# Kernel optimization log

Measured on AMD Instinct MI355X. Metric: run time of the kernel, lower is better.

The kernel has to match this reference:

```python
import jax, jax.numpy as jnp
import numpy as np

B, S, D = 1, 4096, 2048
H, KV, HD = 16, 4, 128
GROUPS = H // KV
SCALE = HD ** -0.5
ROPE_BASE = 10000.0
NEG = -1e9


def _rope_tables():
    inv_freq = 1.0 / (ROPE_BASE ** (jnp.arange(0, HD, 2, dtype=jnp.float32) / HD))  # [HD/2]
    pos = jnp.arange(S, dtype=jnp.float32)
    freqs = pos[:, None] * inv_freq[None, :]            # [S, HD/2]
    emb = jnp.concatenate([freqs, freqs], axis=-1)      # [S, HD] (HF convention)
    return jnp.cos(emb)[None], jnp.sin(emb)[None]       # [1, S, HD]


def setup_inputs() -> dict:
    key = jax.random.key(0)
    ks = jax.random.split(key, 6)
    cos, sin = _rope_tables()
    causal = jnp.tril(jnp.ones((S, S), dtype=bool))
    attention_mask = jnp.where(causal, 0.0, NEG).astype(jnp.float32)[None, None]  # [1,1,S,S]
    std = 0.02
    return {
        "hidden_states": jax.random.normal(ks[0], (B, S, D), jnp.float32),
        "cos": cos.astype(jnp.float32),
        "sin": sin.astype(jnp.float32),
        "attention_mask": attention_mask,
        "wq": jax.random.normal(ks[1], (H * HD, D), jnp.float32) * std,
        "wk": jax.random.normal(ks[2], (KV * HD, D), jnp.float32) * std,
        "wv": jax.random.normal(ks[3], (KV * HD, D), jnp.float32) * std,
        "wo": jax.random.normal(ks[4], (D, H * HD), jnp.float32) * std,
    }


def _rotate_half(x):
    x1, x2 = x[..., : HD // 2], x[..., HD // 2:]
    return jnp.concatenate([-x2, x1], axis=-1)


def reference(hidden_states, cos, sin, attention_mask, wq, wk, wv, wo):
    b, s, _ = hidden_states.shape
    # projections -> [B, n_heads, S, HD]
    q = (hidden_states @ wq.T).reshape(b, s, H, HD).transpose(0, 2, 1, 3)
    k = (hidden_states @ wk.T).reshape(b, s, KV, HD).transpose(0, 2, 1, 3)
    v = (hidden_states @ wv.T).reshape(b, s, KV, HD).transpose(0, 2, 1, 3)
    # RoPE (HF apply_rotary_pos_emb, unsqueeze head dim)
    c, sn = cos[:, None], sin[:, None]
    q = q * c + _rotate_half(q) * sn
    k = k * c + _rotate_half(k) * sn
    # GQA: repeat kv heads
    k = jnp.repeat(k, GROUPS, axis=1)
    v = jnp.repeat(v, GROUPS, axis=1)
    # eager attention
    scores = jnp.einsum("bhqd,bhkd->bhqk", q, k) * SCALE + attention_mask
    attn = jax.nn.softmax(scores, axis=-1)
    out = jnp.einsum("bhqk,bhkd->bhqd", attn, v)
    out = out.transpose(0, 2, 1, 3).reshape(b, s, H * HD)
    # output projection (all-reduce is identity at world_size=1)
    return out @ wo.T
```

## Files before the change

kernel.cpp:

```cpp
#include <hip/hip_runtime.h>
#include <hip/hip_bf16.h>

#define SEQ   4096
#define DMODEL 2048
#define NHEAD 16
#define NKVH  4
#define HDIM  128
#define NQ    (NHEAD*HDIM)
#define NKV   (NKVH*HDIM)
#define NQKV  (NQ + 2*NKV)
#define SCALE 0.08838834764831845f
#define LOG2E 1.4426950408889634f
#define SCL2  (SCALE * LOG2E)

typedef __bf16 bf16x4 __attribute__((ext_vector_type(4)));
typedef __bf16 bf16x8 __attribute__((ext_vector_type(8)));
typedef float  f32x4  __attribute__((ext_vector_type(4)));

#define GLOBAL_CPTR(x) ((const __attribute__((address_space(1))) void*)(x))
#define LDS_PTR(x)     ((__attribute__((address_space(3))) void*)(x))

__global__ __launch_bounds__(256)
void convert_kernel(__bf16* __restrict__ dst, const float* __restrict__ src, int n8)
{
    const int i = blockIdx.x * 256 + threadIdx.x;
    if (i >= n8) return;
    const size_t e0 = (size_t)i * 8;
    const float4 a = *(const float4*)(src + e0);
    const float4 b = *(const float4*)(src + e0 + 4);
    bf16x8 o;
    o[0]=(__bf16)a.x; o[1]=(__bf16)a.y; o[2]=(__bf16)a.z; o[3]=(__bf16)a.w;
    o[4]=(__bf16)b.x; o[5]=(__bf16)b.y; o[6]=(__bf16)b.z; o[7]=(__bf16)b.w;
    *(bf16x8*)(dst + e0) = o;
}

__global__ __launch_bounds__(256)
void gemm_bt(const __bf16* __restrict__ A, const __bf16* __restrict__ Bw,
             void* __restrict__ Cv, __bf16* __restrict__ kb2, __bf16* __restrict__ vt2,
             const float* __restrict__ ct, const float* __restrict__ st,
             int M, int N, int K, int cmode)
{
    __shared__ alignas(16) __bf16 As[2][128*32];
    __shared__ alignas(16) __bf16 Bs[2][128*32];

    const int tid  = threadIdx.x;
    const int w    = tid >> 6;
    const int lane = tid & 63;
    const int l16  = lane & 15;
    const int quad = lane >> 4;
    const int m0 = blockIdx.y * 128;
    const int n0 = blockIdx.x * 128;

    const int srow = lane >> 2;
    const int scol = (lane & 3) * 8;

    const int wm = (w >> 1) * 64;
    int coff[4];
    #pragma unroll
    for (int nt = 0; nt < 4; ++nt)
        coff[nt] = (cmode == 3) ? ((w & 1) * 32 + ((nt & 2) ? 64 : 0) + (nt & 1) * 16)
                                : ((w & 1) * 64 + nt * 16);

    f32x4 acc[4][4];
    #pragma unroll
    for (int mt = 0; mt < 4; ++mt)
        #pragma unroll
        for (int nt = 0; nt < 4; ++nt)
            acc[mt][nt] = (f32x4){0.f, 0.f, 0.f, 0.f};

    auto STAGE = [&](int k0, int b) {
        #pragma unroll
        for (int c = 0; c < 2; ++c) {
            const int r0 = w * 32 + c * 16;
            const __bf16* ga = A + (size_t)(m0 + r0 + srow) * K + k0 + scol;
            __builtin_amdgcn_global_load_lds(GLOBAL_CPTR(ga), LDS_PTR(&As[b][r0 * 32]), 16, 0, 0);
            const __bf16* gb = Bw + (size_t)(n0 + r0 + srow) * K + k0 + scol;
            __builtin_amdgcn_global_load_lds(GLOBAL_CPTR(gb), LDS_PTR(&Bs[b][r0 * 32]), 16, 0, 0);
        }
    };

    STAGE(0, 0);
    for (int k0 = 0; k0 < K; k0 += 32) {
        const int b = (k0 >> 5) & 1;
        __syncthreads();
        if (k0 + 32 < K) STAGE(k0 + 32, b ^ 1);

        bf16x8 af[4], bf[4];
        #pragma unroll
        for (int mt = 0; mt < 4; ++mt)
            af[mt] = *(const bf16x8*)&As[b][(wm + mt*16 + l16) * 32 + quad * 8];
        #pragma unroll
        for (int nt = 0; nt < 4; ++nt)
            bf[nt] = *(const bf16x8*)&Bs[b][(coff[nt] + l16) * 32 + quad * 8];
        __builtin_amdgcn_s_setprio(1);
        #pragma unroll
        for (int mt = 0; mt < 4; ++mt)
            #pragma unroll
            for (int nt = 0; nt < 4; ++nt)
                acc[mt][nt] = __builtin_amdgcn_mfma_f32_16x16x32_bf16(
                    af[mt], bf[nt], acc[mt][nt], 0, 0, 0);
        __builtin_amdgcn_s_setprio(0);
    }

    if (cmode == 3) {
        if (n0 >= 2560) {
            #pragma unroll
            for (int mt = 0; mt < 4; ++mt)
                #pragma unroll
                for (int nt = 0; nt < 4; ++nt) {
                    const int col = (n0 - 2560) + coff[nt] + l16;
                    const int row = m0 + wm + mt*16 + quad*4;
                    bf16x4 pk;
                    #pragma unroll
                    for (int r = 0; r < 4; ++r) pk[r] = (__bf16)acc[mt][nt][r];
                    *(bf16x4*)&vt2[(size_t)col * M + row] = pk;
                }
        } else {
            __bf16* dst;
            int ncols, cb;
            if (n0 < 2048) { dst = (__bf16*)Cv; ncols = NQ;  cb = n0; }
            else           { dst = kb2;         ncols = NKV; cb = n0 - 2048; }
            #pragma unroll
            for (int mt = 0; mt < 4; ++mt)
                #pragma unroll
                for (int np = 0; np < 2; ++np) {
                    const int d = coff[np] + l16;
                    #pragma unroll
                    for (int r = 0; r < 4; ++r) {
                        const int s = m0 + wm + mt*16 + quad*4 + r;
                        const float c  = ct[s * HDIM + d];
                        const float sn = st[s * HDIM + d];
                        const float x1 = acc[mt][np][r];
                        const float x2 = acc[mt][np + 2][r];
                        dst[(size_t)s * ncols + cb + d]      = (__bf16)(x1 * c - x2 * sn);
                        dst[(size_t)s * ncols + cb + d + 64] = (__bf16)(x2 * c + x1 * sn);
                    }
                }
        }
    } else if (cmode == 1) {
        float* Cf = (float*)Cv;
        #pragma unroll
        for (int mt = 0; mt < 4; ++mt)
            #pragma unroll
            for (int nt = 0; nt < 4; ++nt) {
                const int row = m0 + wm + mt*16 + quad*4;
                const int col = n0 + coff[nt] + l16;
                #pragma unroll
                for (int r = 0; r < 4; ++r)
                    Cf[(size_t)(row + r) * N + col] = acc[mt][nt][r];
            }
    } else {
        __bf16* Cb = (__bf16*)Cv;
        #pragma unroll
        for (int mt = 0; mt < 4; ++mt)
            #pragma unroll
            for (int nt = 0; nt < 4; ++nt) {
                const int row = m0 + wm + mt*16 + quad*4;
                const int col = n0 + coff[nt] + l16;
                #pragma unroll
                for (int r = 0; r < 4; ++r)
                    Cb[(size_t)(row + r) * N + col] = (__bf16)acc[mt][nt][r];
            }
    }
}

__global__ __launch_bounds__(512, 4)
void attn_kernel(__bf16* __restrict__ QO, const __bf16* __restrict__ Kb,
                 const __bf16* __restrict__ Vt)
{
    __shared__ alignas(16) __bf16 Klds[2][4][64][32];
    __shared__ alignas(16) __bf16 Vlds[2][2][128][32];
    __shared__ alignas(16) __bf16 Ps[8][16][64];

    const int tid  = threadIdx.x;
    const int w    = tid >> 6;
    const int lane = tid & 63;
    const int l16  = lane & 15;
    const int quad = lane >> 4;
    const int bx = (int)blockIdx.x;
    const int h  = (int)blockIdx.y;
    const int g  = h >> 2;
    const int nbx = (int)gridDim.x;
    const int qt = (h < 8) ? (nbx - 1 - bx) : bx;
    const int m0 = qt * 128;
    const int wrow = m0 + w * 16;

    const int srow = lane >> 2;
    const int scol = (((lane & 3) ^ ((lane >> 3) & 3)) * 8);
    const int rsw  = (quad ^ ((l16 >> 1) & 3)) * 8;

    const int kcw = w & 3;
    const int hw  = w >> 2;

    bf16x8 qf[4];
    {
        const size_t qbase = (size_t)(wrow + l16) * NQ + h * HDIM;
        #pragma unroll
        for (int kc = 0; kc < 4; ++kc)
            qf[kc] = *(const bf16x8*)&QO[qbase + kc * 32 + quad * 8];
    }

    bf16x8 onesf;
    #pragma unroll
    for (int i = 0; i < 8; ++i) onesf[i] = (__bf16)1.0f;

    const __bf16* kSrc = Kb + (size_t)(hw * 32 + srow) * NKV + g * HDIM + kcw * 32 + scol;
    const __bf16* vSrc = Vt + (size_t)(g * HDIM + kcw * 32 + srow) * SEQ + hw * 32 + scol;

    auto STAGE = [&](int jj, int b) {
        const int n0g = jj * 64;
        #pragma unroll
        for (int c = 0; c < 2; ++c) {
            __builtin_amdgcn_global_load_lds(
                GLOBAL_CPTR(kSrc + (size_t)(n0g + c * 16) * NKV),
                LDS_PTR(&Klds[b][kcw][hw * 32 + c * 16][0]), 16, 0, 0);
            __builtin_amdgcn_global_load_lds(
                GLOBAL_CPTR(vSrc + (size_t)(c * 16) * SEQ + n0g),
                LDS_PTR(&Vlds[b][hw][kcw * 32 + c * 16][0]), 16, 0, 0);
        }
    };

    f32x4 lacc = (f32x4){0.f, 0.f, 0.f, 0.f};
    f32x4 oacc[8];
    #pragma unroll
    for (int t = 0; t < 8; ++t) oacc[t] = (f32x4){0.f, 0.f, 0.f, 0.f};

    const int njt = 2 * qt + 2;
    STAGE(0, 0);
    for (int j = 0; j < njt; ++j) {
        __syncthreads();
        if (j + 1 < njt) STAGE(j + 1, (j + 1) & 1);
        const int n0g = j * 64;
        if (n0g > wrow + 15) continue;
        const int b = j & 1;

        f32x4 sacc[4];
        #pragma unroll
        for (int nt = 0; nt < 4; ++nt) sacc[nt] = (f32x4){0.f, 0.f, 0.f, 0.f};
        __builtin_amdgcn_s_setprio(1);
        #pragma unroll
        for (int kc = 0; kc < 4; ++kc) {
            #pragma unroll
            for (int nt = 0; nt < 4; ++nt) {
                const bf16x8 kf = *(const bf16x8*)&Klds[b][kc][nt * 16 + l16][rsw];
                sacc[nt] = __builtin_amdgcn_mfma_f32_16x16x32_bf16(qf[kc], kf, sacc[nt], 0, 0, 0);
            }
        }
        __builtin_amdgcn_s_setprio(0);

        const bool needmask = (n0g + 64 > wrow);
        #pragma unroll
        for (int r = 0; r < 4; ++r) {
            const int qr = wrow + quad * 4 + r;
            const int prow = quad * 4 + r;
            const int pxor = (prow & 7) << 3;
            #pragma unroll
            for (int nt = 0; nt < 4; ++nt) {
                float e = exp2f(sacc[nt][r] * SCL2);
                if (needmask && (n0g + nt * 16 + l16) > qr) e = 0.f;
                Ps[w][prow][(nt * 16 + l16) ^ pxor] = (__bf16)e;
            }
        }

        bf16x8 pa[2];
        #pragma unroll
        for (int kc = 0; kc < 2; ++kc)
            pa[kc] = *(const bf16x8*)&Ps[w][l16][(kc * 32 + quad * 8) ^ ((l16 & 7) << 3)];

        __builtin_amdgcn_s_setprio(1);
        lacc = __builtin_amdgcn_mfma_f32_16x16x32_bf16(pa[0], onesf, lacc, 0, 0, 0);
        lacc = __builtin_amdgcn_mfma_f32_16x16x32_bf16(pa[1], onesf, lacc, 0, 0, 0);
        #pragma unroll
        for (int kc = 0; kc < 2; ++kc)
            #pragma unroll
            for (int t = 0; t < 8; ++t) {
                const bf16x8 vf = *(const bf16x8*)&Vlds[b][kc][t * 16 + l16][rsw];
                oacc[t] = __builtin_amdgcn_mfma_f32_16x16x32_bf16(pa[kc], vf, oacc[t], 0, 0, 0);
            }
        __builtin_amdgcn_s_setprio(0);
    }

    float rinv[4];
    #pragma unroll
    for (int r = 0; r < 4; ++r) rinv[r] = 1.f / lacc[r];
    #pragma unroll
    for (int t = 0; t < 8; ++t)
        #pragma unroll
        for (int r = 0; r < 4; ++r) {
            const int qr = wrow + quad * 4 + r;
            QO[(size_t)qr * NQ + h * HDIM + t * 16 + l16] = (__bf16)(oacc[t][r] * rinv[r]);
        }
}

extern "C" void kernel_launch(void* const* d_in, const int* in_sizes, int n_in,
                              void* d_out, int out_size, void* d_ws, size_t ws_size,
                              hipStream_t stream)
{
    const float* hidden = (const float*)d_in[0];
    const float* cosp   = (const float*)d_in[1];
    const float* sinp   = (const float*)d_in[2];
    const float* wq = (const float*)d_in[4];
    const float* wk = (const float*)d_in[5];
    const float* wv = (const float*)d_in[6];
    const float* wo = (const float*)d_in[7];

    const size_t nw_q = (size_t)NQ  * DMODEL;
    const size_t nw_k = (size_t)NKV * DMODEL;
    const size_t nq_e = (size_t)SEQ * NQ;
    const size_t nk_e = (size_t)SEQ * NKV;

    __bf16* ws     = (__bf16*)d_ws;
    __bf16* wo_b   = ws;
    __bf16* wqkv_b = wo_b + nw_q;
    __bf16* qbuf   = wqkv_b + nw_q + 2 * nw_k;
    __bf16* kbuf   = qbuf + nq_e;
    __bf16* vtb    = kbuf + nk_e;
    __bf16* hbuf   = (__bf16*)d_out;

    const dim3 blk(256);
    convert_kernel<<<dim3(nw_q / 8 / 256), blk, 0, stream>>>(wqkv_b, wq, nw_q / 8);
    convert_kernel<<<dim3(nw_k / 8 / 256), blk, 0, stream>>>(wqkv_b + nw_q, wk, nw_k / 8);
    convert_kernel<<<dim3(nw_k / 8 / 256), blk, 0, stream>>>(wqkv_b + nw_q + nw_k, wv, nw_k / 8);
    convert_kernel<<<dim3(nw_q / 8 / 256), blk, 0, stream>>>(wo_b, wo, nw_q / 8);
    convert_kernel<<<dim3(nq_e / 8 / 256), blk, 0, stream>>>(hbuf, hidden, nq_e / 8);

    gemm_bt<<<dim3(NQKV / 128, SEQ / 128), blk, 0, stream>>>(
        hbuf, wqkv_b, qbuf, kbuf, vtb, cosp, sinp, SEQ, NQKV, DMODEL, 3);

    attn_kernel<<<dim3(SEQ / 128, NHEAD), dim3(512), 0, stream>>>(qbuf, kbuf, vtb);

    gemm_bt<<<dim3(DMODEL / 128, SEQ / 128), blk, 0, stream>>>(
        qbuf, wo_b, d_out, nullptr, nullptr, nullptr, nullptr, SEQ, DMODEL, DMODEL, 1);
}
```

Before: 431.3 us.

## Fuse conversion launches, swizzle GEMM LDS tiles, split attention mask path

Merges the five fp32-to-bf16 conversion launches into one kernel that picks its source and destination from the block index. Adds an XOR swizzle on the GEMM shared-memory staging and fragment reads to reduce LDS bank conflicts. Splits the attention softmax into a masked path for diagonal tiles and an unmasked path for the rest, which removes per-element compare work on most tiles. Drops the unused bf16 GEMM epilogue.

After: 412.7 us. 4.3% less time.

```diff
diff --git a/kernel.cpp b/kernel.cpp
--- a/kernel.cpp
+++ b/kernel.cpp
@@ -21,16 +21,27 @@
 #define LDS_PTR(x)     ((__attribute__((address_space(3))) void*)(x))
 
 __global__ __launch_bounds__(256)
-void convert_kernel(__bf16* __restrict__ dst, const float* __restrict__ src, int n8)
+void convert_all(__bf16* __restrict__ wqkv, __bf16* __restrict__ wob,
+                 __bf16* __restrict__ hb,
+                 const float* __restrict__ wq, const float* __restrict__ wk,
+                 const float* __restrict__ wv, const float* __restrict__ wo,
+                 const float* __restrict__ hid)
 {
-    const int i = blockIdx.x * 256 + threadIdx.x;
-    if (i >= n8) return;
-    const size_t e0 = (size_t)i * 8;
+    const int b = blockIdx.x;
+    const float* src;
+    __bf16* dst;
+    int ib;
+    if (b < 2048)      { src = wq;  dst = wqkv;                                 ib = b; }
+    else if (b < 2560) { src = wk;  dst = wqkv + (size_t)NQ * DMODEL;           ib = b - 2048; }
+    else if (b < 3072) { src = wv;  dst = wqkv + (size_t)(NQ + NKV) * DMODEL;   ib = b - 2560; }
+    else if (b < 5120) { src = wo;  dst = wob;                                  ib = b - 3072; }
+    else               { src = hid; dst = hb;                                   ib = b - 5120; }
+    const size_t e0 = ((size_t)ib * 256 + threadIdx.x) * 8;
     const float4 a = *(const float4*)(src + e0);
-    const float4 b = *(const float4*)(src + e0 + 4);
+    const float4 c = *(const float4*)(src + e0 + 4);
     bf16x8 o;
     o[0]=(__bf16)a.x; o[1]=(__bf16)a.y; o[2]=(__bf16)a.z; o[3]=(__bf16)a.w;
-    o[4]=(__bf16)b.x; o[5]=(__bf16)b.y; o[6]=(__bf16)b.z; o[7]=(__bf16)b.w;
+    o[4]=(__bf16)c.x; o[5]=(__bf16)c.y; o[6]=(__bf16)c.z; o[7]=(__bf16)c.w;
     *(bf16x8*)(dst + e0) = o;
 }
 
@@ -52,7 +63,8 @@
     const int n0 = blockIdx.x * 128;
 
     const int srow = lane >> 2;
-    const int scol = (lane & 3) * 8;
+    const int scol = (((lane & 3) ^ ((lane >> 3) & 3)) * 8);
+    const int rsw  = (quad ^ ((l16 >> 1) & 3)) * 8;
 
     const int wm = (w >> 1) * 64;
     int coff[4];
@@ -88,10 +100,10 @@
         bf16x8 af[4], bf[4];
         #pragma unroll
         for (int mt = 0; mt < 4; ++mt)
-            af[mt] = *(const bf16x8*)&As[b][(wm + mt*16 + l16) * 32 + quad * 8];
+            af[mt] = *(const bf16x8*)&As[b][(wm + mt*16 + l16) * 32 + rsw];
         #pragma unroll
         for (int nt = 0; nt < 4; ++nt)
-            bf[nt] = *(const bf16x8*)&Bs[b][(coff[nt] + l16) * 32 + quad * 8];
+            bf[nt] = *(const bf16x8*)&Bs[b][(coff[nt] + l16) * 32 + rsw];
         __builtin_amdgcn_s_setprio(1);
         #pragma unroll
         for (int mt = 0; mt < 4; ++mt)
@@ -137,7 +149,7 @@
                     }
                 }
         }
-    } else if (cmode == 1) {
+    } else {
         float* Cf = (float*)Cv;
         #pragma unroll
         for (int mt = 0; mt < 4; ++mt)
@@ -148,18 +160,6 @@
                 #pragma unroll
                 for (int r = 0; r < 4; ++r)
                     Cf[(size_t)(row + r) * N + col] = acc[mt][nt][r];
-            }
-    } else {
-        __bf16* Cb = (__bf16*)Cv;
-        #pragma unroll
-        for (int mt = 0; mt < 4; ++mt)
-            #pragma unroll
-            for (int nt = 0; nt < 4; ++nt) {
-                const int row = m0 + wm + mt*16 + quad*4;
-                const int col = n0 + coff[nt] + l16;
-                #pragma unroll
-                for (int r = 0; r < 4; ++r)
-                    Cb[(size_t)(row + r) * N + col] = (__bf16)acc[mt][nt][r];
             }
     }
 }
@@ -248,17 +248,27 @@
         }
         __builtin_amdgcn_s_setprio(0);
 
-        const bool needmask = (n0g + 64 > wrow);
-        #pragma unroll
-        for (int r = 0; r < 4; ++r) {
-            const int qr = wrow + quad * 4 + r;
-            const int prow = quad * 4 + r;
-            const int pxor = (prow & 7) << 3;
-            #pragma unroll
-            for (int nt = 0; nt < 4; ++nt) {
-                float e = exp2f(sacc[nt][r] * SCL2);
-                if (needmask && (n0g + nt * 16 + l16) > qr) e = 0.f;
-                Ps[w][prow][(nt * 16 + l16) ^ pxor] = (__bf16)e;
+        if (n0g + 64 > wrow) {
+            #pragma unroll
+            for (int r = 0; r < 4; ++r) {
+                const int qr = wrow + quad * 4 + r;
+                const int prow = quad * 4 + r;
+                const int pxor = (prow & 7) << 3;
+                #pragma unroll
+                for (int nt = 0; nt < 4; ++nt) {
+                    float e = exp2f(sacc[nt][r] * SCL2);
+                    if ((n0g + nt * 16 + l16) > qr) e = 0.f;
+                    Ps[w][prow][(nt * 16 + l16) ^ pxor] = (__bf16)e;
+                }
+            }
+        } else {
+            #pragma unroll
+            for (int r = 0; r < 4; ++r) {
+                const int prow = quad * 4 + r;
+                const int pxor = (prow & 7) << 3;
+                #pragma unroll
+                for (int nt = 0; nt < 4; ++nt)
+                    Ps[w][prow][(nt * 16 + l16) ^ pxor] = (__bf16)exp2f(sacc[nt][r] * SCL2);
             }
         }
 
@@ -317,18 +327,14 @@
     __bf16* vtb    = kbuf + nk_e;
     __bf16* hbuf   = (__bf16*)d_out;
 
-    const dim3 blk(256);
-    convert_kernel<<<dim3(nw_q / 8 / 256), blk, 0, stream>>>(wqkv_b, wq, nw_q / 8);
-    convert_kernel<<<dim3(nw_k / 8 / 256), blk, 0, stream>>>(wqkv_b + nw_q, wk, nw_k / 8);
-    convert_kernel<<<dim3(nw_k / 8 / 256), blk, 0, stream>>>(wqkv_b + nw_q + nw_k, wv, nw_k / 8);
-    convert_kernel<<<dim3(nw_q / 8 / 256), blk, 0, stream>>>(wo_b, wo, nw_q / 8);
-    convert_kernel<<<dim3(nq_e / 8 / 256), blk, 0, stream>>>(hbuf, hidden, nq_e / 8);
-
-    gemm_bt<<<dim3(NQKV / 128, SEQ / 128), blk, 0, stream>>>(
+    convert_all<<<dim3(9216), dim3(256), 0, stream>>>(
+        wqkv_b, wo_b, hbuf, wq, wk, wv, wo, hidden);
+
+    gemm_bt<<<dim3(NQKV / 128, SEQ / 128), dim3(256), 0, stream>>>(
         hbuf, wqkv_b, qbuf, kbuf, vtb, cosp, sinp, SEQ, NQKV, DMODEL, 3);
 
     attn_kernel<<<dim3(SEQ / 128, NHEAD), dim3(512), 0, stream>>>(qbuf, kbuf, vtb);
 
-    gemm_bt<<<dim3(DMODEL / 128, SEQ / 128), blk, 0, stream>>>(
+    gemm_bt<<<dim3(DMODEL / 128, SEQ / 128), dim3(256), 0, stream>>>(
         qbuf, wo_b, d_out, nullptr, nullptr, nullptr, nullptr, SEQ, DMODEL, DMODEL, 1);
 }
```
